# Optimization experiments

Hardware: AMD Instinct MI355X
Metric: run time of the kernel (lower is better)

Reference implementation:

```python
import jax, jax.numpy as jnp
import numpy as np

B, N, C = 8, 2048, 151  # batch, num rois, n_obj_classes
D_IN = C + 4            # RELPN_WITH_BBOX_INFO adds 4 normalized box coords
HID = 64


def setup_inputs() -> dict:
    key = jax.random.key(0)
    ks = jax.random.split(key, 8)
    # rois: [B, N, 5] = (batch_idx, x1, y1, x2, y2) in pixel coords
    boxes = jax.random.uniform(ks[0], (B, N, 4), dtype=jnp.float32) * 600.0
    rois = jnp.concatenate([jnp.zeros((B, N, 1), jnp.float32), boxes], axis=2)
    roi_feat = jax.random.normal(ks[1], (B, N, C), dtype=jnp.float32)
    im_info = jnp.ones((B, 3), jnp.float32) * 600.0  # (h, w, scale)
    s1 = 1.0 / np.sqrt(D_IN)
    s2 = 1.0 / np.sqrt(HID)
    return {
        "rois": rois,
        "roi_feat": roi_feat,
        "im_info": im_info,
        "w1_sub": jax.random.normal(ks[2], (D_IN, HID), jnp.float32) * s1,
        "b1_sub": jnp.zeros((HID,), jnp.float32),
        "w2_sub": jax.random.normal(ks[3], (HID, HID), jnp.float32) * s2,
        "b2_sub": jnp.zeros((HID,), jnp.float32),
        "w1_obj": jax.random.normal(ks[4], (D_IN, HID), jnp.float32) * s1,
        "b1_obj": jnp.zeros((HID,), jnp.float32),
        "w2_obj": jax.random.normal(ks[5], (HID, HID), jnp.float32) * s2,
        "b2_obj": jnp.zeros((HID,), jnp.float32),
        "K": 2048,
    }


def _mlp(x, w1, b1, w2, b2):
    return jax.nn.relu(x @ w1 + b1) @ w2 + b2


def reference(rois, roi_feat, im_info, w1_sub, b1_sub, w2_sub, b2_sub,
              w1_obj, b1_obj, w2_obj, b2_obj, K):
    b, n, _ = roi_feat.shape
    # normalized bbox info appended to roi features (RELPN_WITH_BBOX_INFO)
    xy = rois[:, :, 1:3] / im_info[:, 1][:, None, None]
    wh = rois[:, :, 3:5] / im_info[:, 0][:, None, None]
    feat = jnp.concatenate([roi_feat, xy, wh], axis=2)  # [B, N, 155]
    feat = jax.lax.stop_gradient(feat)  # original uses roi_feat4prop.detach()
    x_sub = _mlp(feat, w1_sub, b1_sub, w2_sub, b2_sub)  # [B, N, 64]
    x_obj = _mlp(feat, w1_obj, b1_obj, w2_obj, b2_obj)  # [B, N, 64]
    # bilinear pair scores: [B, N, N] -> [B, N*N]
    bil = jnp.einsum("bnd,bmd->bnm", x_sub, x_obj).reshape(b, n * n)
    vis_score = jax.nn.sigmoid(bil)  # [B, N*N]
    # proposal layer: top-K scoring (sub, obj) pairs per image
    top_scores, top_idx = jax.lax.top_k(vis_score, K)  # [B, K]
    sub_idx = top_idx // n
    obj_idx = top_idx % n
    boxes = rois[:, :, 1:5]  # [B, N, 4]
    sub_boxes = jnp.take_along_axis(boxes, sub_idx[:, :, None], axis=1)
    obj_boxes = jnp.take_along_axis(boxes, obj_idx[:, :, None], axis=1)
    roi_pairs = jnp.concatenate([sub_boxes, obj_boxes], axis=2)  # [B, K, 8]
    roi_proposals = jnp.stack([sub_idx, obj_idx], axis=2)        # [B, K, 2]
    return roi_pairs, roi_proposals, top_scores, vis_score
```

## Files before the change

kernel.cpp:

```cpp
#include <hip/hip_runtime.h>
#include <math.h>

#define NB 8
#define NN_ROI 2048
#define C_FEAT 151
#define D_IN 155
#define HID 64
#define K_TOP 2048
#define NN2 (NN_ROI*NN_ROI)
#define CAP 4096
#define NKB 1024
#define SLOTS 131072
#define LCAP 448
#define BM 128
#define BN 128

#define WS_XS    0x0
#define WS_XO    0x400000
#define WS_CNT2  0x800000
#define WS_FLAGS 0x800040
#define WS_CAND2 0x800080
#define WS_NEED  (0x800080 + NB*SLOTS*4)

__global__ __launch_bounds__(256) void mlp_kernel(
    const float* __restrict__ rois, const float* __restrict__ roi_feat,
    const float* __restrict__ im_info,
    const float* __restrict__ w1_sub, const float* __restrict__ b1_sub,
    const float* __restrict__ w2_sub, const float* __restrict__ b2_sub,
    const float* __restrict__ w1_obj, const float* __restrict__ b1_obj,
    const float* __restrict__ w2_obj, const float* __restrict__ b2_obj,
    float* __restrict__ Xs, float* __restrict__ Xo,
    int* __restrict__ cnt2, int* __restrict__ flags)
{
    __shared__ __align__(16) float featL[32][156];
    __shared__ __align__(16) float hL[32][68];
    const int tid   = threadIdx.x;
    const int pass  = blockIdx.x >> 9;
    const int chunk = blockIdx.x & 511;
    const int row0  = chunk * 32;
    const int b     = row0 >> 11;
    const float* w1 = pass ? w1_obj : w1_sub;
    const float* w2 = pass ? w2_obj : w2_sub;
    const float* b1 = pass ? b1_obj : b1_sub;
    const float* b2 = pass ? b2_obj : b2_sub;
    float* X = pass ? Xo : Xs;
    const float im0 = im_info[b*3+0];
    const float im1 = im_info[b*3+1];

    if (blockIdx.x == 0 && tid < 9) {
        if (tid < 8) cnt2[tid] = 0;
        else flags[0] = 0;
    }

    for (int i = tid; i < 32*C_FEAT; i += 256) {
        const int r = i / C_FEAT, d = i - r*C_FEAT;
        featL[r][d] = roi_feat[(size_t)(row0+r)*C_FEAT + d];
    }
    if (tid < 32) {
        const int r = tid;
        #pragma unroll
        for (int c = 0; c < 4; ++c)
            featL[r][C_FEAT+c] = rois[(size_t)(row0+r)*5 + 1 + c] / (c < 2 ? im1 : im0);
    }
    __syncthreads();

    const int tx = tid & 15, ty = tid >> 4;
    float acc[2][4] = {};
    for (int d4 = 0; d4 < 38; ++d4) {
        const int d = d4*4;
        float wv[4][4], fv[2][4];
        #pragma unroll
        for (int q = 0; q < 4; ++q)
            *(float4*)wv[q] = *(const float4*)&w1[(d+q)*HID + tx*4];
        #pragma unroll
        for (int i = 0; i < 2; ++i)
            *(float4*)fv[i] = *(const float4*)&featL[ty*2+i][d];
        #pragma unroll
        for (int q = 0; q < 4; ++q)
            #pragma unroll
            for (int i = 0; i < 2; ++i)
                #pragma unroll
                for (int j = 0; j < 4; ++j)
                    acc[i][j] = fmaf(fv[i][q], wv[q][j], acc[i][j]);
    }
    #pragma unroll
    for (int d = 152; d < 155; ++d) {
        float wv[4];
        *(float4*)wv = *(const float4*)&w1[d*HID + tx*4];
        #pragma unroll
        for (int i = 0; i < 2; ++i) {
            const float f = featL[ty*2+i][d];
            #pragma unroll
            for (int j = 0; j < 4; ++j)
                acc[i][j] = fmaf(f, wv[j], acc[i][j]);
        }
    }
    {
        float b1v[4];
        *(float4*)b1v = *(const float4*)&b1[tx*4];
        #pragma unroll
        for (int i = 0; i < 2; ++i)
            #pragma unroll
            for (int j = 0; j < 4; ++j) {
                const float v = acc[i][j] + b1v[j];
                hL[ty*2+i][tx*4+j] = v > 0.0f ? v : 0.0f;
            }
    }
    __syncthreads();

    float x[2][4] = {};
    for (int k4 = 0; k4 < 16; ++k4) {
        const int k = k4*4;
        float wv[4][4], hv[2][4];
        #pragma unroll
        for (int q = 0; q < 4; ++q)
            *(float4*)wv[q] = *(const float4*)&w2[(k+q)*HID + tx*4];
        #pragma unroll
        for (int i = 0; i < 2; ++i)
            *(float4*)hv[i] = *(const float4*)&hL[ty*2+i][k];
        #pragma unroll
        for (int q = 0; q < 4; ++q)
            #pragma unroll
            for (int i = 0; i < 2; ++i)
                #pragma unroll
                for (int j = 0; j < 4; ++j)
                    x[i][j] = fmaf(hv[i][q], wv[q][j], x[i][j]);
    }
    {
        float b2v[4];
        *(float4*)b2v = *(const float4*)&b2[tx*4];
        #pragma unroll
        for (int i = 0; i < 2; ++i) {
            *(float4*)&X[(size_t)(row0 + ty*2 + i)*HID + tx*4] = make_float4(
                x[i][0]+b2v[0], x[i][1]+b2v[1], x[i][2]+b2v[2], x[i][3]+b2v[3]);
        }
    }
}

__global__ __launch_bounds__(256) void bil_kernel(
    const float* __restrict__ Xs, const float* __restrict__ Xo,
    float* __restrict__ vis, int* __restrict__ cnt2,
    unsigned int* __restrict__ cand2, int* __restrict__ flags)
{
    __shared__ __align__(16) float As[16][128];
    __shared__ __align__(16) float Bs[16][128];
    __shared__ unsigned int lcand[LCAP];
    __shared__ int lcnt, lbase;
    const int tid = threadIdx.x;
    const int tx = tid & 15, ty = tid >> 4;
    const int bm = blockIdx.x * BM, bn = blockIdx.y * BN, b = blockIdx.z;
    if (tid == 0) lcnt = 0;

    const float4* Ag = (const float4*)(Xs + ((size_t)b*NN_ROI + bm)*HID);
    const float4* Bg = (const float4*)(Xo + ((size_t)b*NN_ROI + bn)*HID);

    float acc[8][8];
    #pragma unroll
    for (int i = 0; i < 8; ++i)
        #pragma unroll
        for (int j = 0; j < 8; ++j) acc[i][j] = 0.0f;

    for (int ph = 0; ph < 4; ++ph) {
        if (ph) __syncthreads();
        #pragma unroll
        for (int it = 0; it < 2; ++it) {
            const int lin = it*256 + tid;
            const int r = lin >> 2, k4 = lin & 3;
            const float4 v = Ag[r*16 + ph*4 + k4];
            const int rs = r ^ (k4 << 3);
            As[k4*4+0][rs] = v.x; As[k4*4+1][rs] = v.y;
            As[k4*4+2][rs] = v.z; As[k4*4+3][rs] = v.w;
        }
        #pragma unroll
        for (int it = 0; it < 2; ++it) {
            const int lin = it*256 + tid;
            const int r = lin >> 2, k4 = lin & 3;
            const float4 v = Bg[r*16 + ph*4 + k4];
            const int rs = r ^ (k4 << 3);
            Bs[k4*4+0][rs] = v.x; Bs[k4*4+1][rs] = v.y;
            Bs[k4*4+2][rs] = v.z; Bs[k4*4+3][rs] = v.w;
        }
        __syncthreads();
        #pragma unroll
        for (int k = 0; k < 16; ++k) {
            const int swz = (k >> 2) << 3;
            const int am = (ty*8) ^ swz;
            const float4 a0 = *(const float4*)&As[k][am];
            const float4 a1 = *(const float4*)&As[k][am + 4];
            const float4 q0 = *(const float4*)&Bs[k][(tx*4) ^ swz];
            const float4 q1 = *(const float4*)&Bs[k][(64 + tx*4) ^ swz];
            const float a[8]  = {a0.x,a0.y,a0.z,a0.w,a1.x,a1.y,a1.z,a1.w};
            const float bb[8] = {q0.x,q0.y,q0.z,q0.w,q1.x,q1.y,q1.z,q1.w};
            #pragma unroll
            for (int i = 0; i < 8; ++i)
                #pragma unroll
                for (int j = 0; j < 8; ++j)
                    acc[i][j] = fmaf(a[i], bb[j], acc[i][j]);
        }
    }

    const size_t visbase = (size_t)b * NN2;
    #pragma unroll
    for (int i = 0; i < 8; ++i) {
        const int row = bm + ty*8 + i;
        float f[8];
        #pragma unroll
        for (int j = 0; j < 8; ++j) {
            const float xv = acc[i][j];
            const float e = __expf(-xv);
            f[j] = __builtin_amdgcn_rcpf(1.0f + e);
            if (xv >= 9.0f) {
                const float se = 1.0f / (1.0f + e);
                const int ku = 0x3F800000 - __float_as_int(se);
                if (ku < NKB) {
                    const int col = bn + (j < 4 ? tx*4 + j : 64 + tx*4 + (j-4));
                    const unsigned int key =
                        ((unsigned int)ku << 22) | (unsigned int)(row*NN_ROI + col);
                    const int p = atomicAdd(&lcnt, 1);
                    if (p < LCAP) lcand[p] = key;
                    else {
                        const int gp = atomicAdd(&cnt2[b], 1);
                        if (gp < SLOTS) cand2[(size_t)b*SLOTS + gp] = key;
                    }
                }
            }
        }
        *(float4*)&vis[visbase + (size_t)row*NN_ROI + bn + tx*4] =
            make_float4(f[0], f[1], f[2], f[3]);
        *(float4*)&vis[visbase + (size_t)row*NN_ROI + bn + 64 + tx*4] =
            make_float4(f[4], f[5], f[6], f[7]);
    }
    __syncthreads();
    int n = lcnt; if (n > LCAP) n = LCAP;
    if (tid == 0) lbase = atomicAdd(&cnt2[b], n);
    __syncthreads();
    const int bs = lbase;
    for (int i = tid; i < n; i += 256) {
        const int p = bs + i;
        if (p < SLOTS) cand2[(size_t)b*SLOTS + p] = lcand[i];
    }
}

__global__ __launch_bounds__(1024) void topk_kernel(
    const int* __restrict__ cnt2, const unsigned int* __restrict__ cand2,
    const float* __restrict__ rois,
    float* __restrict__ pairs, float* __restrict__ props, float* __restrict__ scores,
    int* __restrict__ flags)
{
    __shared__ unsigned int key[CAP];
    __shared__ int hist[NKB];
    __shared__ int part[64];
    __shared__ int scnt;
    __shared__ int kTsh;
    const int b = blockIdx.x, tid = threadIdx.x;
    int M = cnt2[b]; if (M > SLOTS) M = SLOTS;
    if (cnt2[b] > SLOTS) atomicOr(flags, 4);

    for (int i = tid; i < NKB; i += 1024) hist[i] = 0;
    if (tid == 0) scnt = 0;
    __syncthreads();
    for (int i = tid; i < M; i += 1024)
        atomicAdd(&hist[cand2[(size_t)b*SLOTS + i] >> 22], 1);
    __syncthreads();
    if (tid < 64) {
        int s = 0;
        for (int i = 0; i < 16; ++i) s += hist[tid*16 + i];
        part[tid] = s;
    }
    __syncthreads();
    if (tid == 0) {
        int cum = 0, kT = NKB - 1; bool found = false;
        for (int c = 0; c < 64; ++c) {
            if (cum + part[c] >= K_TOP) {
                for (int i = c*16; i < c*16 + 16; ++i) {
                    cum += hist[i];
                    if (cum >= K_TOP) { kT = i; found = true; break; }
                }
                break;
            }
            cum += part[c];
        }
        if (!found) atomicOr(flags, 16);
        kTsh = kT;
    }
    __syncthreads();
    const unsigned long long kl = ((unsigned long long)(kTsh + 1)) << 22;
    for (int c = tid; c < CAP; c += 1024) key[c] = 0xFFFFFFFFu;
    __syncthreads();
    for (int i = tid; i < M; i += 1024) {
        const unsigned int k = cand2[(size_t)b*SLOTS + i];
        if ((unsigned long long)k < kl) {
            const int p = atomicAdd(&scnt, 1);
            if (p < CAP) key[p] = k;
        }
    }
    __syncthreads();
    if (tid == 0) {
        if (scnt < K_TOP) atomicOr(flags, 2);
        if (scnt > CAP)   atomicOr(flags, 4);
    }
    for (int kk = 2; kk <= CAP; kk <<= 1)
        for (int j = kk >> 1; j > 0; j >>= 1) {
            for (int t = tid; t < CAP/2; t += 1024) {
                const int i = 2*t - (t & (j-1));
                const int p = i + j;
                const bool up = (i & kk) == 0;
                const unsigned int a = key[i], c2 = key[p];
                if (up ? (a > c2) : (a < c2)) { key[i] = c2; key[p] = a; }
            }
            __syncthreads();
        }
    for (int k = tid; k < K_TOP-1; k += 1024)
        if (key[k] >= key[k+1]) atomicOr(flags, 8);
    for (int k = tid; k < K_TOP; k += 1024) {
        const unsigned int kw = key[k];
        const int idx = (int)(kw & 0x3FFFFFu);
        const int ku  = (int)(kw >> 22);
        const int sub = idx >> 11, obj = idx & (NN_ROI-1);
        const float sc = __int_as_float(0x3F800000 - ku);
        const float* rs = rois + ((size_t)b*NN_ROI + sub)*5 + 1;
        const float* ro = rois + ((size_t)b*NN_ROI + obj)*5 + 1;
        const size_t o = (size_t)b*K_TOP + k;
        *(float4*)&pairs[o*8]   = make_float4(rs[0],rs[1],rs[2],rs[3]);
        *(float4*)&pairs[o*8+4] = make_float4(ro[0],ro[1],ro[2],ro[3]);
        props[o*2]   = (float)sub;
        props[o*2+1] = (float)obj;
        scores[o]    = sc;
    }
}

__global__ void check_kernel(const int* __restrict__ flags, float* __restrict__ pairs)
{
    const int f = *flags;
    if (f) pairs[0] = 1e5f * (float)f;
}

__global__ void sentinel_kernel(float* out) { out[0] = 1e5f; }

extern "C" void kernel_launch(void* const* d_in, const int* in_sizes, int n_in,
                              void* d_out, int out_size, void* d_ws, size_t ws_size,
                              hipStream_t stream)
{
    static const int EXP_SIZES[12] = {81920, 2473984, 24, 9920, 64, 4096, 64,
                                      9920, 64, 4096, 64, 1};
    bool ok = (n_in == 12) && (out_size == 33734656) && (ws_size >= (size_t)WS_NEED);
    if (ok) for (int i = 0; i < 12; ++i) if (in_sizes[i] != EXP_SIZES[i]) { ok = false; break; }
    if (!ok) { sentinel_kernel<<<1, 1, 0, stream>>>((float*)d_out); return; }

    const float* rois     = (const float*)d_in[0];
    const float* roi_feat = (const float*)d_in[1];
    const float* im_info  = (const float*)d_in[2];
    const float* w1_sub   = (const float*)d_in[3];
    const float* b1_sub   = (const float*)d_in[4];
    const float* w2_sub   = (const float*)d_in[5];
    const float* b2_sub   = (const float*)d_in[6];
    const float* w1_obj   = (const float*)d_in[7];
    const float* b1_obj   = (const float*)d_in[8];
    const float* w2_obj   = (const float*)d_in[9];
    const float* b2_obj   = (const float*)d_in[10];

    char* ws = (char*)d_ws;
    float* Xs           = (float*)(ws + WS_XS);
    float* Xo           = (float*)(ws + WS_XO);
    int* cnt2           = (int*)  (ws + WS_CNT2);
    int* flags          = (int*)  (ws + WS_FLAGS);
    unsigned int* cand2 = (unsigned int*)(ws + WS_CAND2);

    float* out    = (float*)d_out;
    float* pairs  = out;
    float* props  = out + 131072;
    float* scores = out + 163840;
    float* vis    = out + 180224;

    mlp_kernel<<<1024, 256, 0, stream>>>(rois, roi_feat, im_info,
        w1_sub, b1_sub, w2_sub, b2_sub, w1_obj, b1_obj, w2_obj, b2_obj,
        Xs, Xo, cnt2, flags);
    bil_kernel<<<dim3(16, 16, NB), 256, 0, stream>>>(Xs, Xo, vis, cnt2, cand2, flags);
    topk_kernel<<<NB, 1024, 0, stream>>>(cnt2, cand2, rois, pairs, props, scores, flags);
    check_kernel<<<1, 1, 0, stream>>>(flags, pairs);
}
```

Baseline: 157.8 us.

## Transpose features into scratch and restructure MLP with wave-uniform weight loads

Adds a kernel that transposes the ROI features plus normalized box coords into a column-major buffer, placed temporarily in the vis output region. The MLP kernel then gives each lane one row and each wave a 16-column slice chosen by a wave-uniform offset, so the weight reads can become scalar loads and the per-row feature reads coalesce. The aim is to remove the shared-memory feature staging and per-thread vector weight loads. In exchange it adds an extra kernel launch and a full global write-then-read of the transposed features.

Result: no change. 159.4 us (+1.0%).

```diff
diff --git a/kernel.cpp b/kernel.cpp
--- a/kernel.cpp
+++ b/kernel.cpp
@@ -8,6 +8,7 @@
 #define HID 64
 #define K_TOP 2048
 #define NN2 (NN_ROI*NN_ROI)
+#define NROWS (NB*NN_ROI)
 #define CAP 4096
 #define NKB 1024
 #define SLOTS 131072
@@ -22,119 +23,91 @@
 #define WS_CAND2 0x800080
 #define WS_NEED  (0x800080 + NB*SLOTS*4)
 
+__global__ __launch_bounds__(256) void featT_kernel(
+    const float* __restrict__ rois, const float* __restrict__ roi_feat,
+    const float* __restrict__ im_info, float* __restrict__ featT,
+    int* __restrict__ cnt2, int* __restrict__ flags)
+{
+    __shared__ float tile[64][153];
+    const int tid = threadIdx.x;
+    const int row0 = blockIdx.x * 64;
+    if (blockIdx.x == 0 && tid < 9) {
+        if (tid < 8) cnt2[tid] = 0;
+        else flags[0] = 0;
+    }
+    for (int i = tid; i < 64*C_FEAT; i += 256) {
+        const int r = i / C_FEAT, d = i - r*C_FEAT;
+        tile[r][d] = roi_feat[(size_t)(row0+r)*C_FEAT + d];
+    }
+    __syncthreads();
+    const int lane = tid & 63, dg = tid >> 6;
+    for (int d = dg; d < C_FEAT; d += 4)
+        featT[(size_t)d*NROWS + row0 + lane] = tile[lane][d];
+    if (dg == 0) {
+        const int b = (row0 + lane) >> 11;
+        const float im0 = im_info[b*3+0], im1 = im_info[b*3+1];
+        #pragma unroll
+        for (int c = 0; c < 4; ++c)
+            featT[(size_t)(C_FEAT+c)*NROWS + row0 + lane] =
+                rois[(size_t)(row0+lane)*5 + 1 + c] / (c < 2 ? im1 : im0);
+    }
+}
+
 __global__ __launch_bounds__(256) void mlp_kernel(
-    const float* __restrict__ rois, const float* __restrict__ roi_feat,
-    const float* __restrict__ im_info,
+    const float* __restrict__ featT,
     const float* __restrict__ w1_sub, const float* __restrict__ b1_sub,
     const float* __restrict__ w2_sub, const float* __restrict__ b2_sub,
     const float* __restrict__ w1_obj, const float* __restrict__ b1_obj,
     const float* __restrict__ w2_obj, const float* __restrict__ b2_obj,
-    float* __restrict__ Xs, float* __restrict__ Xo,
-    int* __restrict__ cnt2, int* __restrict__ flags)
-{
-    __shared__ __align__(16) float featL[32][156];
-    __shared__ __align__(16) float hL[32][68];
+    float* __restrict__ Xs, float* __restrict__ Xo)
+{
+    __shared__ float hL[64][65];
     const int tid   = threadIdx.x;
-    const int pass  = blockIdx.x >> 9;
-    const int chunk = blockIdx.x & 511;
-    const int row0  = chunk * 32;
-    const int b     = row0 >> 11;
+    const int lane  = tid & 63;
+    const int c0    = __builtin_amdgcn_readfirstlane((tid >> 6) << 4);
+    const int pass  = blockIdx.x >> 8;
+    const int chunk = blockIdx.x & 255;
+    const int row   = chunk*64 + lane;
     const float* w1 = pass ? w1_obj : w1_sub;
     const float* w2 = pass ? w2_obj : w2_sub;
     const float* b1 = pass ? b1_obj : b1_sub;
     const float* b2 = pass ? b2_obj : b2_sub;
     float* X = pass ? Xo : Xs;
-    const float im0 = im_info[b*3+0];
-    const float im1 = im_info[b*3+1];
-
-    if (blockIdx.x == 0 && tid < 9) {
-        if (tid < 8) cnt2[tid] = 0;
-        else flags[0] = 0;
-    }
-
-    for (int i = tid; i < 32*C_FEAT; i += 256) {
-        const int r = i / C_FEAT, d = i - r*C_FEAT;
-        featL[r][d] = roi_feat[(size_t)(row0+r)*C_FEAT + d];
-    }
-    if (tid < 32) {
-        const int r = tid;
-        #pragma unroll
-        for (int c = 0; c < 4; ++c)
-            featL[r][C_FEAT+c] = rois[(size_t)(row0+r)*5 + 1 + c] / (c < 2 ? im1 : im0);
-    }
-    __syncthreads();
-
-    const int tx = tid & 15, ty = tid >> 4;
-    float acc[2][4] = {};
-    for (int d4 = 0; d4 < 38; ++d4) {
-        const int d = d4*4;
-        float wv[4][4], fv[2][4];
-        #pragma unroll
-        for (int q = 0; q < 4; ++q)
-            *(float4*)wv[q] = *(const float4*)&w1[(d+q)*HID + tx*4];
-        #pragma unroll
-        for (int i = 0; i < 2; ++i)
-            *(float4*)fv[i] = *(const float4*)&featL[ty*2+i][d];
-        #pragma unroll
-        for (int q = 0; q < 4; ++q)
-            #pragma unroll
-            for (int i = 0; i < 2; ++i)
-                #pragma unroll
-                for (int j = 0; j < 4; ++j)
-                    acc[i][j] = fmaf(fv[i][q], wv[q][j], acc[i][j]);
-    }
-    #pragma unroll
-    for (int d = 152; d < 155; ++d) {
-        float wv[4];
-        *(float4*)wv = *(const float4*)&w1[d*HID + tx*4];
-        #pragma unroll
-        for (int i = 0; i < 2; ++i) {
-            const float f = featL[ty*2+i][d];
-            #pragma unroll
-            for (int j = 0; j < 4; ++j)
-                acc[i][j] = fmaf(f, wv[j], acc[i][j]);
-        }
-    }
-    {
-        float b1v[4];
-        *(float4*)b1v = *(const float4*)&b1[tx*4];
-        #pragma unroll
-        for (int i = 0; i < 2; ++i)
-            #pragma unroll
-            for (int j = 0; j < 4; ++j) {
-                const float v = acc[i][j] + b1v[j];
-                hL[ty*2+i][tx*4+j] = v > 0.0f ? v : 0.0f;
-            }
-    }
-    __syncthreads();
-
-    float x[2][4] = {};
-    for (int k4 = 0; k4 < 16; ++k4) {
-        const int k = k4*4;
-        float wv[4][4], hv[2][4];
-        #pragma unroll
-        for (int q = 0; q < 4; ++q)
-            *(float4*)wv[q] = *(const float4*)&w2[(k+q)*HID + tx*4];
-        #pragma unroll
-        for (int i = 0; i < 2; ++i)
-            *(float4*)hv[i] = *(const float4*)&hL[ty*2+i][k];
-        #pragma unroll
-        for (int q = 0; q < 4; ++q)
-            #pragma unroll
-            for (int i = 0; i < 2; ++i)
-                #pragma unroll
-                for (int j = 0; j < 4; ++j)
-                    x[i][j] = fmaf(hv[i][q], wv[q][j], x[i][j]);
-    }
-    {
-        float b2v[4];
-        *(float4*)b2v = *(const float4*)&b2[tx*4];
-        #pragma unroll
-        for (int i = 0; i < 2; ++i) {
-            *(float4*)&X[(size_t)(row0 + ty*2 + i)*HID + tx*4] = make_float4(
-                x[i][0]+b2v[0], x[i][1]+b2v[1], x[i][2]+b2v[2], x[i][3]+b2v[3]);
-        }
-    }
+
+    float acc[16];
+    #pragma unroll
+    for (int j = 0; j < 16; ++j) acc[j] = 0.0f;
+    #pragma unroll 5
+    for (int d = 0; d < D_IN; ++d) {
+        const float f = featT[(size_t)d*NROWS + chunk*64 + lane];
+        const float* wr = w1 + d*HID + c0;
+        #pragma unroll
+        for (int j = 0; j < 16; ++j)
+            acc[j] = fmaf(f, wr[j], acc[j]);
+    }
+    #pragma unroll
+    for (int j = 0; j < 16; ++j) {
+        const float v = acc[j] + b1[c0 + j];
+        hL[lane][c0 + j] = v > 0.0f ? v : 0.0f;
+    }
+    __syncthreads();
+    float x[16];
+    #pragma unroll
+    for (int j = 0; j < 16; ++j) x[j] = 0.0f;
+    #pragma unroll 4
+    for (int k = 0; k < HID; ++k) {
+        const float hv = hL[lane][k];
+        const float* w2r = w2 + k*HID + c0;
+        #pragma unroll
+        for (int j = 0; j < 16; ++j)
+            x[j] = fmaf(hv, w2r[j], x[j]);
+    }
+    float* Xr = X + (size_t)row*HID + c0;
+    #pragma unroll
+    for (int j4 = 0; j4 < 4; ++j4)
+        *(float4*)&Xr[j4*4] = make_float4(
+            x[j4*4+0]+b2[c0+j4*4+0], x[j4*4+1]+b2[c0+j4*4+1],
+            x[j4*4+2]+b2[c0+j4*4+2], x[j4*4+3]+b2[c0+j4*4+3]);
 }
 
 __global__ __launch_bounds__(256) void bil_kernel(
@@ -371,10 +344,12 @@
     float* props  = out + 131072;
     float* scores = out + 163840;
     float* vis    = out + 180224;
-
-    mlp_kernel<<<1024, 256, 0, stream>>>(rois, roi_feat, im_info,
-        w1_sub, b1_sub, w2_sub, b2_sub, w1_obj, b1_obj, w2_obj, b2_obj,
-        Xs, Xo, cnt2, flags);
+    float* featT  = vis;
+
+    featT_kernel<<<256, 256, 0, stream>>>(rois, roi_feat, im_info, featT,
+                                          cnt2, flags);
+    mlp_kernel<<<512, 256, 0, stream>>>(featT,
+        w1_sub, b1_sub, w2_sub, b2_sub, w1_obj, b1_obj, w2_obj, b2_obj, Xs, Xo);
     bil_kernel<<<dim3(16, 16, NB), 256, 0, stream>>>(Xs, Xo, vis, cnt2, cand2, flags);
     topk_kernel<<<NB, 1024, 0, stream>>>(cnt2, cand2, rois, pairs, props, scores, flags);
     check_kernel<<<1, 1, 0, stream>>>(flags, pairs);
```
